# Kernel tuning notes

Measured on AMD Instinct MI355X. Metric: run time of the kernel, lower is better.

Reference implementation:

```python
import jax, jax.numpy as jnp
import numpy as np

N = 1_000_000
B = 8
C_FEAT = 32
C_TIME = 32
C_IN = C_FEAT + C_TIME
C_OUT = 64
K = 27  # 3^3 kernel offsets
BN_EPS = 1e-5


def setup_inputs() -> dict:
    key = jax.random.key(0)
    ks = jax.random.split(key, 8)
    feats = jax.random.normal(ks[0], (N, C_FEAT), dtype=jnp.float32)
    time_emb = jax.random.normal(ks[1], (B, C_TIME), dtype=jnp.float32)
    W = jax.random.normal(ks[2], (K, C_IN, C_OUT), dtype=jnp.float32) / np.sqrt(C_IN * K)
    bias = jax.random.normal(ks[3], (C_OUT,), dtype=jnp.float32) * 0.01
    gamma = jnp.ones((C_OUT,), dtype=jnp.float32)
    beta = jnp.zeros((C_OUT,), dtype=jnp.float32)
    batch_idx = jnp.sort(jax.random.randint(ks[4], (N,), 0, B, dtype=jnp.int32))
    nbr_idx = jax.random.randint(ks[5], (K, N), 0, N, dtype=jnp.int32)
    nbr_valid = jax.random.randint(ks[6], (K, N), 0, 2, dtype=jnp.int32)
    return {"feats": feats, "time_emb": time_emb, "W": W, "bias": bias,
            "gamma": gamma, "beta": beta, "batch_idx": batch_idx,
            "nbr_idx": nbr_idx, "nbr_valid": nbr_valid}


def reference(feats, time_emb, W, bias, gamma, beta, batch_idx, nbr_idx, nbr_valid):
    # --- ME.cat((x, time_emb_sparse)): broadcast per-batch embedding to points ---
    x = jnp.concatenate([feats, time_emb[batch_idx]], axis=-1)  # [N, C_IN]

    # --- MinkowskiConvolution: per-offset gather -> GEMM -> accumulate ---
    valid_f = nbr_valid.astype(x.dtype)  # [K, N]

    def step(acc, kw):
        w, idx, valid = kw  # [C_IN,C_OUT], [N], [N]
        g = x[idx] * valid[:, None]        # gather + mask, [N, C_IN]
        return acc + g @ w, None

    out0 = jnp.zeros((x.shape[0], W.shape[-1]), x.dtype)
    out, _ = jax.lax.scan(step, out0, (W, nbr_idx, valid_f))
    out = out + bias  # [N, C_OUT]

    # --- MinkowskiBatchNorm (training-mode batch stats over all points) ---
    mean = out.mean(axis=0)
    var = ((out - mean) ** 2).mean(axis=0)
    y = (out - mean) * jax.lax.rsqrt(var + BN_EPS) * gamma + beta

    # --- MinkowskiSiLU ---
    return y * jax.nn.sigmoid(y)
```

## Files before the change

### kernel.cpp

```cpp
#include <hip/hip_runtime.h>

#define NPTS 1000000
#define KOFF 27
#define CONV_BLOCK 512
#define ROWS_PER_BLOCK 256
#define NWG_CONV 3907
#define NWAVES (NWG_CONV * 8)

typedef __bf16 bf16x8 __attribute__((ext_vector_type(8)));
typedef __bf16 bf16x4 __attribute__((ext_vector_type(4)));
typedef float f32x4 __attribute__((ext_vector_type(4)));

__global__ __launch_bounds__(256) void build_xh_kernel(
    const float* __restrict__ feats, __bf16* __restrict__ xh)
{
    const long g = (long)blockIdx.x * 256 + threadIdx.x;
    if (g >= (long)NPTS * 8) return;
    const int row = (int)(g >> 3);
    const int c = ((int)g & 7) << 2;
    f32x4 v = __builtin_nontemporal_load((const f32x4*)(feats + (size_t)row * 32 + c));
    bf16x4 o;
    o[0] = (__bf16)v[0]; o[1] = (__bf16)v[1];
    o[2] = (__bf16)v[2]; o[3] = (__bf16)v[3];
    *(bf16x4*)(xh + (size_t)row * 32 + c) = o;
}

__global__ __launch_bounds__(256) void prep_kernel(
    const float* __restrict__ W, const float* __restrict__ time_emb,
    const int* __restrict__ batch_idx,
    __bf16* __restrict__ wlo, __bf16* __restrict__ twc, int* __restrict__ bounds)
{
    const int b = blockIdx.x;
    if (b < 216) {
        const int g = b * 256 + threadIdx.x;
        const int k = g >> 11, rem = g & 2047;
        const int co = rem >> 5, ci = rem & 31;
        wlo[g] = (__bf16)W[k * 4096 + ci * 64 + co];
    } else if (b < 270) {
        const int g = (b - 216) * 256 + threadIdx.x;
        if (g >= KOFF * 512) return;
        const int k = g >> 9, rem = g & 511;
        const int co = rem >> 3, slot = rem & 7;
        float v = 0.f;
#pragma unroll
        for (int ci = 0; ci < 32; ++ci)
            v += time_emb[slot * 32 + ci] * W[k * 4096 + (32 + ci) * 64 + co];
        twc[g] = (__bf16)v;
    } else {
        const int j = threadIdx.x;
        if (j > 8) return;
        if (j == 0) { bounds[0] = 0; return; }
        if (j == 8) { bounds[8] = NPTS; return; }
        int lo = 0, hi = NPTS;
        while (lo < hi) {
            const int mid = (lo + hi) >> 1;
            if (batch_idx[mid] < j) lo = mid + 1; else hi = mid;
        }
        bounds[j] = lo;
    }
}

__device__ __forceinline__ int batch_of(int g, int t1, int t2, int t3, int t4,
                                        int t5, int t6, int t7)
{
    return (g >= t1) + (g >= t2) + (g >= t3) + (g >= t4) +
           (g >= t5) + (g >= t6) + (g >= t7);
}

template <int BF16PRE>
__global__ __launch_bounds__(CONV_BLOCK, 2) void conv_kernel(
    const __bf16* __restrict__ xh, const int* __restrict__ bounds,
    const __bf16* __restrict__ wlo, const __bf16* __restrict__ twc,
    const int* __restrict__ nbr_idx, const int* __restrict__ nbr_valid,
    float* __restrict__ outf, __bf16* __restrict__ pre,
    float* __restrict__ partials)
{
    __shared__ __bf16 w_lds[KOFF * 2048];

    const int tid  = threadIdx.x;
    const int wave = tid >> 6;
    const int lane = tid & 63;
    const int l15  = lane & 15;
    const int quad = lane >> 4;
    const int R0   = blockIdx.x * ROWS_PER_BLOCK + wave * 32;
    const int row0 = R0 + l15;
    const int row1 = row0 + 16;
    const bool ok0 = row0 < NPTS;
    const bool ok1 = row1 < NPTS;
    const int r0c = ok0 ? row0 : NPTS - 1;
    const int r1c = ok1 ? row1 : NPTS - 1;

    {
        const bf16x8* src = (const bf16x8*)wlo;
        bf16x8* dst = (bf16x8*)w_lds;
#pragma unroll
        for (int i = 0; i < 14; ++i) {
            const int c = tid + i * CONV_BLOCK;
            if (c < 6912) dst[c] = src[c];
        }
    }
    __syncthreads();

    const int t1 = __builtin_amdgcn_readfirstlane(bounds[1]);
    const int t2 = __builtin_amdgcn_readfirstlane(bounds[2]);
    const int t3 = __builtin_amdgcn_readfirstlane(bounds[3]);
    const int t4 = __builtin_amdgcn_readfirstlane(bounds[4]);
    const int t5 = __builtin_amdgcn_readfirstlane(bounds[5]);
    const int t6 = __builtin_amdgcn_readfirstlane(bounds[6]);
    const int t7 = __builtin_amdgcn_readfirstlane(bounds[7]);

    f32x4 acc[2][4];
#pragma unroll
    for (int m = 0; m < 2; ++m)
#pragma unroll
        for (int ct = 0; ct < 4; ++ct)
            acc[m][ct] = (f32x4){0.f, 0.f, 0.f, 0.f};

    bf16x8 X0[5], X1[5];
    int M0[5], M1[5];
    bf16x8 tf[5][4];
    int ii0[9], ii1[9], vv0[9], vv1[9];

    const bf16x8 zero8 = {};

#pragma unroll
    for (int s = 0; s < 8; ++s) {
        const long kb = (long)s * NPTS;
        ii0[s] = __builtin_nontemporal_load(nbr_idx + kb + r0c);
        ii1[s] = __builtin_nontemporal_load(nbr_idx + kb + r1c);
        vv0[s] = __builtin_nontemporal_load(nbr_valid + kb + r0c);
        vv1[s] = __builtin_nontemporal_load(nbr_valid + kb + r1c);
    }
#pragma unroll
    for (int s = 0; s < 4; ++s) {
        const bf16x8* tk = (const bf16x8*)twc + s * 64;
        if (quad == 0) {
#pragma unroll
            for (int ct = 0; ct < 4; ++ct) tf[s][ct] = tk[ct * 16 + l15];
        } else {
#pragma unroll
            for (int ct = 0; ct < 4; ++ct) tf[s][ct] = zero8;
        }
        const int g0 = ii0[s], g1 = ii1[s];
        const bool va0 = vv0[s] && ok0;
        const bool va1 = vv1[s] && ok1;
        bf16x8 x0 = zero8, x1 = zero8;
        if (va0) x0 = *(const bf16x8*)(xh + (size_t)g0 * 32 + quad * 8);
        if (va1) x1 = *(const bf16x8*)(xh + (size_t)g1 * 32 + quad * 8);
        X0[s] = x0; X1[s] = x1;
        M0[s] = va0 ? batch_of(g0, t1, t2, t3, t4, t5, t6, t7) : 8;
        M1[s] = va1 ? batch_of(g1, t1, t2, t3, t4, t5, t6, t7) : 8;
    }

    const __bf16 onebf = (__bf16)1.0f;
    const __bf16 zbf   = (__bf16)0.0f;

#pragma unroll
    for (int j = 0; j < KOFF; ++j) {
        if (j + 4 < KOFF) {
            const int s = (j + 4) % 5;
            const bf16x8* tk = (const bf16x8*)twc + (j + 4) * 64;
            if (quad == 0) {
#pragma unroll
                for (int ct = 0; ct < 4; ++ct) tf[s][ct] = tk[ct * 16 + l15];
            } else {
#pragma unroll
                for (int ct = 0; ct < 4; ++ct) tf[s][ct] = zero8;
            }
            const int si = (j + 4) % 9;
            const int g0 = ii0[si], g1 = ii1[si];
            const bool va0 = vv0[si] && ok0;
            const bool va1 = vv1[si] && ok1;
            bf16x8 x0 = zero8, x1 = zero8;
            if (va0) x0 = *(const bf16x8*)(xh + (size_t)g0 * 32 + quad * 8);
            if (va1) x1 = *(const bf16x8*)(xh + (size_t)g1 * 32 + quad * 8);
            X0[s] = x0; X1[s] = x1;
            M0[s] = va0 ? batch_of(g0, t1, t2, t3, t4, t5, t6, t7) : 8;
            M1[s] = va1 ? batch_of(g1, t1, t2, t3, t4, t5, t6, t7) : 8;
        }

        if (j + 8 < KOFF) {
            const int si = (j + 8) % 9;
            const long kb = (long)(j + 8) * NPTS;
            ii0[si] = __builtin_nontemporal_load(nbr_idx + kb + r0c);
            ii1[si] = __builtin_nontemporal_load(nbr_idx + kb + r1c);
            vv0[si] = __builtin_nontemporal_load(nbr_valid + kb + r0c);
            vv1[si] = __builtin_nontemporal_load(nbr_valid + kb + r1c);
        }

        bf16x8 wf[4];
        {
            const bf16x8* wk = (const bf16x8*)w_lds + j * 256;
#pragma unroll
            for (int ct = 0; ct < 4; ++ct)
                wf[ct] = wk[(ct * 16 + l15) * 4 + quad];
        }
        const int s = j % 5;
        const int m0 = (quad == 0) ? M0[s] : 8;
        const int m1 = (quad == 0) ? M1[s] : 8;
        bf16x8 oh0, oh1;
#pragma unroll
        for (int jj = 0; jj < 8; ++jj) {
            oh0[jj] = (m0 == jj) ? onebf : zbf;
            oh1[jj] = (m1 == jj) ? onebf : zbf;
        }
#pragma unroll
        for (int ct = 0; ct < 4; ++ct) {
            acc[0][ct] = __builtin_amdgcn_mfma_f32_16x16x32_bf16(wf[ct], X0[s], acc[0][ct], 0, 0, 0);
            acc[1][ct] = __builtin_amdgcn_mfma_f32_16x16x32_bf16(wf[ct], X1[s], acc[1][ct], 0, 0, 0);
            acc[0][ct] = __builtin_amdgcn_mfma_f32_16x16x32_bf16(tf[s][ct], oh0, acc[0][ct], 0, 0, 0);
            acc[1][ct] = __builtin_amdgcn_mfma_f32_16x16x32_bf16(tf[s][ct], oh1, acc[1][ct], 0, 0, 0);
        }
    }

#pragma unroll
    for (int m = 0; m < 2; ++m) {
        const int p = R0 + m * 16 + l15;
        if (p < NPTS) {
            if (BF16PRE) {
                __bf16* pp = pre + (size_t)p * 64 + quad * 4;
#pragma unroll
                for (int ct = 0; ct < 4; ++ct) {
                    const f32x4 a = acc[m][ct];
                    bf16x4 o;
                    o[0] = (__bf16)a[0]; o[1] = (__bf16)a[1];
                    o[2] = (__bf16)a[2]; o[3] = (__bf16)a[3];
                    *(bf16x4*)(pp + ct * 16) = o;
                }
            } else {
                float* pp = outf + (size_t)p * 64 + quad * 4;
#pragma unroll
                for (int ct = 0; ct < 4; ++ct)
                    *(f32x4*)(pp + ct * 16) = acc[m][ct];
            }
        }
    }

    const size_t pb = ((size_t)blockIdx.x * 8 + wave) * 128;
#pragma unroll
    for (int ct = 0; ct < 4; ++ct) {
        f32x4 sv, qv;
#pragma unroll
        for (int j = 0; j < 4; ++j) {
            float s  = acc[0][ct][j] + acc[1][ct][j];
            float ss = acc[0][ct][j] * acc[0][ct][j] + acc[1][ct][j] * acc[1][ct][j];
            s += __shfl_xor(s, 1);  ss += __shfl_xor(ss, 1);
            s += __shfl_xor(s, 2);  ss += __shfl_xor(ss, 2);
            s += __shfl_xor(s, 4);  ss += __shfl_xor(ss, 4);
            s += __shfl_xor(s, 8);  ss += __shfl_xor(ss, 8);
            sv[j] = s; qv[j] = ss;
        }
        if (l15 == 0) {
            *(f32x4*)(partials + pb + ct * 16 + quad * 4)      = sv;
            *(f32x4*)(partials + pb + 64 + ct * 16 + quad * 4) = qv;
        }
    }
}

__global__ __launch_bounds__(256) void bn_pass1(
    const float* __restrict__ partials, float* __restrict__ p2)
{
    __shared__ float lds[256];
    const int tid = threadIdx.x;
    const int c = tid & 127;
    const int half = tid >> 7;
    float s = 0.f;
    for (int r = blockIdx.x * 2 + half; r < NWAVES; r += 256)
        s += __builtin_nontemporal_load(partials + (size_t)r * 128 + c);
    lds[tid] = s;
    __syncthreads();
    if (tid < 128) p2[blockIdx.x * 128 + tid] = lds[tid] + lds[tid + 128];
}

__global__ void bn_pass2(const float* __restrict__ p2, const float* __restrict__ gamma,
                         const float* __restrict__ beta, float* __restrict__ bn)
{
    __shared__ float lds[128];
    const int t = threadIdx.x;
    float s = 0.f;
    for (int b = 0; b < 128; ++b) s += p2[b * 128 + t];
    lds[t] = s;
    __syncthreads();
    if (t < 64) {
        const float inv_n = 1.0f / (float)NPTS;
        const float mean = lds[t] * inv_n;
        const float var = lds[t + 64] * inv_n - mean * mean;
        const float scale = rsqrtf(var + 1e-5f) * gamma[t];
        bn[t] = scale;
        bn[64 + t] = beta[t] - mean * scale;
    }
}

__global__ __launch_bounds__(256) void bn_silu_bf16_kernel(
    const __bf16* __restrict__ pre, float* __restrict__ out, const float* __restrict__ bn)
{
    __shared__ float s[128];
    if (threadIdx.x < 128) s[threadIdx.x] = bn[threadIdx.x];
    __syncthreads();
    const long M8 = (long)NPTS * 8;
    for (long i = (long)blockIdx.x * 256 + threadIdx.x; i < M8; i += (long)gridDim.x * 256) {
        const int c0 = ((int)i & 7) << 3;
        const bf16x8 v = __builtin_nontemporal_load((const bf16x8*)pre + i);
        f32x4 lo, hi;
#pragma unroll
        for (int j = 0; j < 4; ++j) {
            const float y = (float)v[j] * s[c0 + j] + s[64 + c0 + j];
            lo[j] = y * (1.0f / (1.0f + __expf(-y)));
        }
#pragma unroll
        for (int j = 0; j < 4; ++j) {
            const float y = (float)v[4 + j] * s[c0 + 4 + j] + s[64 + c0 + 4 + j];
            hi[j] = y * (1.0f / (1.0f + __expf(-y)));
        }
        f32x4* o = (f32x4*)out + i * 2;
        o[0] = lo; o[1] = hi;
    }
}

__global__ __launch_bounds__(256) void bn_silu_f32_kernel(
    float* __restrict__ out, const float* __restrict__ bn)
{
    __shared__ float s[128];
    if (threadIdx.x < 128) s[threadIdx.x] = bn[threadIdx.x];
    __syncthreads();
    f32x4* o4 = (f32x4*)out;
    const long M4 = (long)NPTS * 16;
    for (long i = (long)blockIdx.x * 256 + threadIdx.x; i < M4; i += (long)gridDim.x * 256) {
        const int c0 = ((int)i & 15) << 2;
        f32x4 v = __builtin_nontemporal_load(o4 + i);
#pragma unroll
        for (int j = 0; j < 4; ++j) {
            const float y = v[j] * s[c0 + j] + s[64 + c0 + j];
            v[j] = y * (1.0f / (1.0f + __expf(-y)));
        }
        o4[i] = v;
    }
}

extern "C" void kernel_launch(void* const* d_in, const int* in_sizes, int n_in,
                              void* d_out, int out_size, void* d_ws, size_t ws_size,
                              hipStream_t stream)
{
    const float* feats     = (const float*)d_in[0];
    const float* time_emb  = (const float*)d_in[1];
    const float* W         = (const float*)d_in[2];
    const float* gamma     = (const float*)d_in[4];
    const float* beta      = (const float*)d_in[5];
    const int*   batch_idx = (const int*)d_in[6];
    const int*   nbr_idx   = (const int*)d_in[7];
    const int*   nbr_valid = (const int*)d_in[8];
    float* out = (float*)d_out;

    char* ws = (char*)d_ws;
    size_t off = 0;
    auto take = [&](size_t bytes) { char* p = ws + off; off = (off + bytes + 255) & ~(size_t)255; return p; };
    __bf16* xh      = (__bf16*)take((size_t)NPTS * 32 * 2);
    int* bounds     = (int*)take(9 * 4);
    __bf16* wlo     = (__bf16*)take((size_t)KOFF * 2048 * 2);
    __bf16* twc     = (__bf16*)take((size_t)KOFF * 512 * 2);
    float* partials = (float*)take((size_t)NWAVES * 128 * 4);
    float* p2       = (float*)take(128 * 128 * 4);
    float* bn       = (float*)take(512);
    const size_t pre_bytes = (size_t)NPTS * 64 * 2;
    const bool bf16pre = (off + pre_bytes) <= ws_size;
    __bf16* pre = bf16pre ? (__bf16*)take(pre_bytes) : (__bf16*)0;

    hipLaunchKernelGGL(build_xh_kernel, dim3(31250), dim3(256), 0, stream, feats, xh);
    hipLaunchKernelGGL(prep_kernel, dim3(271), dim3(256), 0, stream,
                       W, time_emb, batch_idx, wlo, twc, bounds);
    if (bf16pre) {
        hipLaunchKernelGGL((conv_kernel<1>), dim3(NWG_CONV), dim3(CONV_BLOCK), 0, stream,
                           xh, bounds, wlo, twc, nbr_idx, nbr_valid, out, pre, partials);
    } else {
        hipLaunchKernelGGL((conv_kernel<0>), dim3(NWG_CONV), dim3(CONV_BLOCK), 0, stream,
                           xh, bounds, wlo, twc, nbr_idx, nbr_valid, out, pre, partials);
    }
    hipLaunchKernelGGL(bn_pass1, dim3(128), dim3(256), 0, stream, partials, p2);
    hipLaunchKernelGGL(bn_pass2, dim3(1), dim3(128), 0, stream, p2, gamma, beta, bn);
    if (bf16pre) {
        hipLaunchKernelGGL(bn_silu_bf16_kernel, dim3(2048), dim3(256), 0, stream, pre, out, bn);
    } else {
        hipLaunchKernelGGL(bn_silu_f32_kernel, dim3(2048), dim3(256), 0, stream, out, bn);
    }
}
```

Baseline: 572.1 us.

## Stage conv weights in two LDS halves and move time-embedding fragments to LDS

Splits the per-block LDS weight buffer into two halves of 14 offsets, reloading the second half mid-loop behind a pair of barriers. This cuts LDS use per block so four 512-thread blocks can share a CU instead of two. The time-embedding weight fragments now come from LDS each iteration instead of a 5-deep register ring filled from global memory, which frees registers for the higher occupancy target. In exchange it adds two block-wide syncs, a second weight staging pass, and more LDS reads per offset.

```diff
diff --git a/kernel.cpp b/kernel.cpp
--- a/kernel.cpp
+++ b/kernel.cpp
@@ -2,6 +2,7 @@
 
 #define NPTS 1000000
 #define KOFF 27
+#define KHALF 14
 #define CONV_BLOCK 512
 #define ROWS_PER_BLOCK 256
 #define NWG_CONV 3907
@@ -68,14 +69,15 @@
 }
 
 template <int BF16PRE>
-__global__ __launch_bounds__(CONV_BLOCK, 2) void conv_kernel(
+__global__ __launch_bounds__(CONV_BLOCK, 4) void conv_kernel(
     const __bf16* __restrict__ xh, const int* __restrict__ bounds,
     const __bf16* __restrict__ wlo, const __bf16* __restrict__ twc,
     const int* __restrict__ nbr_idx, const int* __restrict__ nbr_valid,
     float* __restrict__ outf, __bf16* __restrict__ pre,
     float* __restrict__ partials)
 {
-    __shared__ __bf16 w_lds[KOFF * 2048];
+    __shared__ __bf16 w_lds[KHALF * 2048];
+    __shared__ __bf16 t_lds[KHALF * 512];
 
     const int tid  = threadIdx.x;
     const int wave = tid >> 6;
@@ -90,15 +92,24 @@
     const int r0c = ok0 ? row0 : NPTS - 1;
     const int r1c = ok1 ? row1 : NPTS - 1;
 
-    {
-        const bf16x8* src = (const bf16x8*)wlo;
-        bf16x8* dst = (bf16x8*)w_lds;
-#pragma unroll
-        for (int i = 0; i < 14; ++i) {
+    auto stage = [&](int k0, int cnt) {
+        const bf16x8* wsrc = (const bf16x8*)wlo + (size_t)k0 * 256;
+        bf16x8* wdst = (bf16x8*)w_lds;
+#pragma unroll
+        for (int i = 0; i < 7; ++i) {
             const int c = tid + i * CONV_BLOCK;
-            if (c < 6912) dst[c] = src[c];
-        }
-    }
+            if (c < cnt * 256) wdst[c] = wsrc[c];
+        }
+        const bf16x8* tsrc = (const bf16x8*)twc + (size_t)k0 * 64;
+        bf16x8* tdst = (bf16x8*)t_lds;
+#pragma unroll
+        for (int i = 0; i < 2; ++i) {
+            const int c = tid + i * CONV_BLOCK;
+            if (c < cnt * 64) tdst[c] = tsrc[c];
+        }
+    };
+
+    stage(0, KHALF);
     __syncthreads();
 
     const int t1 = __builtin_amdgcn_readfirstlane(bounds[1]);
@@ -118,7 +129,6 @@
 
     bf16x8 X0[5], X1[5];
     int M0[5], M1[5];
-    bf16x8 tf[5][4];
     int ii0[9], ii1[9], vv0[9], vv1[9];
 
     const bf16x8 zero8 = {};
@@ -133,14 +143,6 @@
     }
 #pragma unroll
     for (int s = 0; s < 4; ++s) {
-        const bf16x8* tk = (const bf16x8*)twc + s * 64;
-        if (quad == 0) {
-#pragma unroll
-            for (int ct = 0; ct < 4; ++ct) tf[s][ct] = tk[ct * 16 + l15];
-        } else {
-#pragma unroll
-            for (int ct = 0; ct < 4; ++ct) tf[s][ct] = zero8;
-        }
         const int g0 = ii0[s], g1 = ii1[s];
         const bool va0 = vv0[s] && ok0;
         const bool va1 = vv1[s] && ok1;
@@ -157,16 +159,14 @@
 
 #pragma unroll
     for (int j = 0; j < KOFF; ++j) {
+        if (j == KHALF) {
+            __syncthreads();
+            stage(KHALF, KOFF - KHALF);
+            __syncthreads();
+        }
+
         if (j + 4 < KOFF) {
             const int s = (j + 4) % 5;
-            const bf16x8* tk = (const bf16x8*)twc + (j + 4) * 64;
-            if (quad == 0) {
-#pragma unroll
-                for (int ct = 0; ct < 4; ++ct) tf[s][ct] = tk[ct * 16 + l15];
-            } else {
-#pragma unroll
-                for (int ct = 0; ct < 4; ++ct) tf[s][ct] = zero8;
-            }
             const int si = (j + 4) % 9;
             const int g0 = ii0[si], g1 = ii1[si];
             const bool va0 = vv0[si] && ok0;
@@ -188,13 +188,24 @@
             vv1[si] = __builtin_nontemporal_load(nbr_valid + kb + r1c);
         }
 
+        const int kk = (j < KHALF) ? j : (j - KHALF);
         bf16x8 wf[4];
         {
-            const bf16x8* wk = (const bf16x8*)w_lds + j * 256;
+            const bf16x8* wk = (const bf16x8*)w_lds + kk * 256;
 #pragma unroll
             for (int ct = 0; ct < 4; ++ct)
                 wf[ct] = wk[(ct * 16 + l15) * 4 + quad];
         }
+        bf16x8 tf[4];
+        if (quad == 0) {
+            const bf16x8* tk = (const bf16x8*)t_lds + kk * 64;
+#pragma unroll
+            for (int ct = 0; ct < 4; ++ct) tf[ct] = tk[ct * 16 + l15];
+        } else {
+#pragma unroll
+            for (int ct = 0; ct < 4; ++ct) tf[ct] = zero8;
+        }
+
         const int s = j % 5;
         const int m0 = (quad == 0) ? M0[s] : 8;
         const int m1 = (quad == 0) ? M1[s] : 8;
@@ -208,8 +219,8 @@
         for (int ct = 0; ct < 4; ++ct) {
             acc[0][ct] = __builtin_amdgcn_mfma_f32_16x16x32_bf16(wf[ct], X0[s], acc[0][ct], 0, 0, 0);
             acc[1][ct] = __builtin_amdgcn_mfma_f32_16x16x32_bf16(wf[ct], X1[s], acc[1][ct], 0, 0, 0);
-            acc[0][ct] = __builtin_amdgcn_mfma_f32_16x16x32_bf16(tf[s][ct], oh0, acc[0][ct], 0, 0, 0);
-            acc[1][ct] = __builtin_amdgcn_mfma_f32_16x16x32_bf16(tf[s][ct], oh1, acc[1][ct], 0, 0, 0);
+            acc[0][ct] = __builtin_amdgcn_mfma_f32_16x16x32_bf16(tf[ct], oh0, acc[0][ct], 0, 0, 0);
+            acc[1][ct] = __builtin_amdgcn_mfma_f32_16x16x32_bf16(tf[ct], oh1, acc[1][ct], 0, 0, 0);
         }
     }
 
```

After: 1.463 ms. 2.56x slower.
